# Optimization experiments

Hardware: AMD Instinct MI355X
Metric: run time of the kernel (lower is better)

Reference implementation:

```python
import jax, jax.numpy as jnp
import numpy as np


def setup_inputs() -> dict:
    key = jax.random.key(0)
    B, D, F = 8192, 768, 32768
    k_x, k_w = jax.random.split(key, 2)
    x = jax.random.normal(k_x, (B, D), dtype=jnp.float32)
    # xavier_normal init for W_enc: std = sqrt(2/(fan_in+fan_out))
    scale = (2.0 / (D + F)) ** 0.5
    W_enc = jax.random.normal(k_w, (D, F), dtype=jnp.float32) * scale
    # W_dec = W_enc.T with unit-norm rows (latent directions)
    W_dec = W_enc.T
    W_dec = W_dec / jnp.linalg.norm(W_dec, axis=1, keepdims=True)
    pre_bias = jnp.zeros((D,), dtype=jnp.float32)
    latent_bias = jnp.zeros((F,), dtype=jnp.float32)
    return {"x": x, "pre_bias": pre_bias, "W_enc": W_enc,
            "latent_bias": latent_bias, "W_dec": W_dec, "k": 32}


def reference(x, pre_bias, W_enc, latent_bias, W_dec, k):
    # encode: [B,F]
    latents_pre_act = (x - pre_bias) @ W_enc + latent_bias
    # topk selection then relu: relu(topk(pre_act, k))
    vals, idx = jax.lax.top_k(latents_pre_act, k)      # [B,k]
    vals = jax.nn.relu(vals)
    # sparse decode: gather only the k selected decoder rows per example
    # W_dec[idx]: [B,k,D]
    recons = jnp.einsum('bk,bkd->bd', vals, W_dec[idx]) + pre_bias
    return recons
```

## Files before the change

### kernel.cpp

```cpp
#include <hip/hip_runtime.h>
#include <stdint.h>

#define GAS __attribute__((address_space(1)))
#define LAS __attribute__((address_space(3)))

typedef __attribute__((ext_vector_type(8))) short bf16x8;
typedef __attribute__((ext_vector_type(4))) float f32x4;

static constexpr int NB = 8192;
static constexpr int DD = 768;
static constexpr int FF = 32768;
static constexpr int TK = 32;
static constexpr int RUNC = 48;
static constexpr int SLOT = 8;
static constexpr int NSEG = FF / 128;
static constexpr int SORTN = 1024;
static constexpr int NS2 = 256;
static constexpr int NKT = DD / 32;
static constexpr int PQ = 256 * 32;

__device__ __forceinline__ ushort f2bf(float f) {
    unsigned x = __float_as_uint(f);
    unsigned r = (x + 0x7FFFu + ((x >> 16) & 1u)) >> 16;
    return (ushort)r;
}
__device__ __forceinline__ ushort sortkey(ushort u) {
    return (u & 0x8000u) ? (ushort)(u ^ 0xFFFFu) : (ushort)(u | 0x8000u);
}
__device__ __forceinline__ float bf2f(ushort u) {
    return __uint_as_float(((unsigned)u) << 16);
}
__device__ __forceinline__ void gload_lds16(const void* g, void* l) {
    __builtin_amdgcn_global_load_lds((const GAS unsigned int*)g,
                                     (LAS unsigned int*)l, 16, 0, 0);
}
__device__ __forceinline__ size_t pan_off(int v, int d) {
    return ((size_t)(v >> 8) * NKT + (d >> 5)) * PQ + ((v & 255) << 5) + (d & 31);
}

__global__ __launch_bounds__(256) void prep_x_k(const float* __restrict__ x,
                                                const float* __restrict__ pb,
                                                ushort* __restrict__ Ap) {
    const int n4 = NB * DD / 4;
    for (int i = blockIdx.x * 256 + threadIdx.x; i < n4; i += gridDim.x * 256) {
        int b = i / (DD / 4), dq = (i % (DD / 4)) * 4;
        float4 v = ((const float4*)x)[i];
        float4 p = ((const float4*)pb)[i % (DD / 4)];
        ushort4 o;
        o.x = f2bf(v.x - p.x); o.y = f2bf(v.y - p.y);
        o.z = f2bf(v.z - p.z); o.w = f2bf(v.w - p.w);
        *(ushort4*)(Ap + pan_off(b, dq)) = o;
    }
}

__global__ __launch_bounds__(256) void prep_w_k(const float* __restrict__ W,
                                                ushort* __restrict__ Bp,
                                                float* __restrict__ Wt32,
                                                float* __restrict__ s2part) {
    __shared__ float tile[32][33];
    int f0 = blockIdx.x * 32, d0 = blockIdx.y * 32;
    int tx = threadIdx.x & 31, ty = threadIdx.x >> 5;
    float ss = 0.f;
#pragma unroll
    for (int q = 0; q < 4; q++) {
        int dl = ty + q * 8;
        float v = W[(size_t)(d0 + dl) * FF + f0 + tx];
        tile[dl][tx] = v;
        ss += v * v;
    }
#pragma unroll
    for (int o = 32; o >= 1; o >>= 1) ss += __shfl_down(ss, o);
    if ((threadIdx.x & 63) == 0) {
        int slot = (blockIdx.x * 97 + blockIdx.y * 13 + (threadIdx.x >> 6)) & (NS2 - 1);
        atomicAdd(&s2part[slot], ss);
    }
    __syncthreads();
#pragma unroll
    for (int q = 0; q < 4; q++) {
        int fl = ty + q * 8;
        float v = tile[tx][fl];
        int f = f0 + fl, d = d0 + tx;
        Bp[pan_off(f, d)] = f2bf(v);
        if (Wt32) Wt32[(size_t)f * DD + d] = v;
    }
}

__global__ __launch_bounds__(256) void rn_k(const float* __restrict__ x,
                                            const float* __restrict__ pb,
                                            const float* __restrict__ s2part,
                                            float* __restrict__ tau) {
    int t = threadIdx.x, l = t & 63, w = t >> 6;
    __shared__ float wsum[4];
    __shared__ float s2m;
    float p = s2part[t];
#pragma unroll
    for (int o = 32; o >= 1; o >>= 1) p += __shfl_down(p, o);
    if (l == 0) wsum[w] = p;
    __syncthreads();
    if (t == 0) s2m = (wsum[0] + wsum[1] + wsum[2] + wsum[3]) / ((float)DD * (float)FF);
    __syncthreads();
    int row = blockIdx.x * 4 + w;
    float ss = 0.f;
#pragma unroll
    for (int q = 0; q < 12; q++) {
        int d = l + 64 * q;
        float v = x[(size_t)row * DD + d] - pb[d];
        ss += v * v;
    }
#pragma unroll
    for (int o = 32; o >= 1; o >>= 1) ss += __shfl_down(ss, o);
    if (l == 0) tau[row] = 2.5f * sqrtf(s2m * ss);
}

__global__ __launch_bounds__(512, 2) void gemm_k(const ushort* __restrict__ Ap,
                                                 const ushort* __restrict__ Bp,
                                                 const float* __restrict__ lbias,
                                                 const float* __restrict__ tau,
                                                 unsigned* __restrict__ cand,
                                                 unsigned* __restrict__ rowbad) {
    __shared__ __align__(16) char smem[98304];

    int bid = (int)blockIdx.x;
    int wg = (bid & 7) * 512 + (bid >> 3);
    int mt = wg >> 7, nt = wg & 127;
    int m0 = mt << 8, n0 = nt << 8;

    int t = threadIdx.x, l = t & 63, w = t >> 6;
    int wm = w >> 2, wn = w & 3;

    const ushort* sA = Ap + (size_t)mt * NKT * PQ + t * 8;
    const ushort* sB = Bp + (size_t)nt * NKT * PQ + t * 8;
    int ldA = t * 16, ldB = 16384 + t * 16;

    int aro = (wm * 128 + (l & 15)) * 64 + ((l >> 4) << 4);
    int bro = (wn * 64 + (l & 15)) * 64 + ((l >> 4) << 4);

    f32x4 acc[8][4] = {};

#define STAGE(slot, kt)                                                       \
    {                                                                         \
        const size_t o = (size_t)(kt) * PQ;                                   \
        char* base = smem + (slot) * 32768;                                   \
        gload_lds16(sA + o, base + ldA);                                      \
        gload_lds16(sA + o + 4096, base + ldA + 8192);                        \
        gload_lds16(sB + o, base + ldB);                                      \
        gload_lds16(sB + o + 4096, base + ldB + 8192);                        \
    }

    STAGE(0, 0)
    STAGE(1, 1)
    asm volatile("s_waitcnt vmcnt(4)" ::: "memory");
    __builtin_amdgcn_s_barrier();
    __builtin_amdgcn_sched_barrier(0);

    int cur = 0;
#pragma unroll 1
    for (int kt = 0; kt < NKT; kt++) {
        const char* As = smem + cur * 32768;
        const char* Bs = As + 16384;
        int nxt = cur + 2; if (nxt >= 3) nxt -= 3;
        if (kt < NKT - 2) STAGE(nxt, kt + 2)

        bf16x8 af[4], bfr[4];
        af[0]  = *(const bf16x8*)(As + aro);
        af[1]  = *(const bf16x8*)(As + aro + 1024);
        af[2]  = *(const bf16x8*)(As + aro + 2048);
        af[3]  = *(const bf16x8*)(As + aro + 3072);
        bfr[0] = *(const bf16x8*)(Bs + bro);
        bfr[1] = *(const bf16x8*)(Bs + bro + 1024);
        bfr[2] = *(const bf16x8*)(Bs + bro + 2048);
        bfr[3] = *(const bf16x8*)(Bs + bro + 3072);
        asm volatile("s_waitcnt lgkmcnt(0)" ::: "memory");
        __builtin_amdgcn_sched_barrier(0);
        __builtin_amdgcn_s_setprio(1);
#pragma unroll
        for (int mi = 0; mi < 4; mi++)
#pragma unroll
            for (int ni = 0; ni < 4; ni++)
                acc[mi][ni] = __builtin_amdgcn_mfma_f32_16x16x32_bf16(
                    af[mi], bfr[ni], acc[mi][ni], 0, 0, 0);
        __builtin_amdgcn_s_setprio(0);
        __builtin_amdgcn_sched_barrier(0);

        af[0] = *(const bf16x8*)(As + aro + 4096);
        af[1] = *(const bf16x8*)(As + aro + 5120);
        af[2] = *(const bf16x8*)(As + aro + 6144);
        af[3] = *(const bf16x8*)(As + aro + 7168);
        asm volatile("s_waitcnt lgkmcnt(0)" ::: "memory");
        __builtin_amdgcn_sched_barrier(0);
        __builtin_amdgcn_s_setprio(1);
#pragma unroll
        for (int mi = 0; mi < 4; mi++)
#pragma unroll
            for (int ni = 0; ni < 4; ni++)
                acc[mi + 4][ni] = __builtin_amdgcn_mfma_f32_16x16x32_bf16(
                    af[mi], bfr[ni], acc[mi + 4][ni], 0, 0, 0);
        __builtin_amdgcn_s_setprio(0);
        __builtin_amdgcn_sched_barrier(0);

        if (kt < NKT - 2)
            asm volatile("s_waitcnt vmcnt(4)" ::: "memory");
        else
            asm volatile("s_waitcnt vmcnt(0)" ::: "memory");
        __builtin_amdgcn_s_barrier();
        __builtin_amdgcn_sched_barrier(0);
        cur = cur + 1; if (cur == 3) cur = 0;
    }
#undef STAGE

    __syncthreads();
    int* lcnt = (int*)smem;
    unsigned* lbuf = (unsigned*)(smem + 2048);
    lcnt[t] = 0;
    __syncthreads();
    float lbv[4]; int fcol[4];
#pragma unroll
    for (int ni = 0; ni < 4; ni++) {
        fcol[ni] = n0 + wn * 64 + ni * 16 + (l & 15);
        lbv[ni] = lbias[fcol[ni]];
    }
    int sh = wn >> 1;
#pragma unroll
    for (int mi = 0; mi < 8; mi++) {
        int rl = wm * 128 + mi * 16 + ((l >> 4) << 2);
        float4 tq = *(const float4*)(tau + m0 + rl);
        float tj[4] = {tq.x, tq.y, tq.z, tq.w};
#pragma unroll
        for (int ni = 0; ni < 4; ni++) {
            f32x4 v4 = acc[mi][ni];
#pragma unroll
            for (int j = 0; j < 4; j++) {
                float v = v4[j] + lbv[ni];
                if (v >= tj[j]) {
                    int idx = ((rl + j) << 1) + sh;
                    int p = atomicAdd(&lcnt[idx], 1);
                    if (p < SLOT)
                        lbuf[idx * SLOT + p] =
                            ((unsigned)sortkey(f2bf(v)) << 16) | (unsigned)(32767 - fcol[ni]);
                }
            }
        }
    }
    __syncthreads();
    {
        int row = t >> 1, sh2 = t & 1;
        int c = lcnt[t];
        int gr = m0 + row;
        if (c > SLOT) { atomicOr(&rowbad[gr], 1u); c = SLOT; }
        unsigned* dstc = cand + (size_t)gr * (NSEG * SLOT) + ((nt << 1) + sh2) * SLOT;
        for (int s2 = 0; s2 < c; s2++) dstc[s2] = lbuf[t * SLOT + s2];
    }
}

__global__ __launch_bounds__(256) void select2_k(const unsigned* __restrict__ cand,
                                                 const unsigned* __restrict__ rowbad,
                                                 unsigned* __restrict__ flagv,
                                                 int* __restrict__ ridx,
                                                 int* __restrict__ runcnt) {
    int b = blockIdx.x, t = threadIdx.x;
    __shared__ unsigned srt[SORTN];
    __shared__ int s_cnt;
    for (int i = t; i < SORTN; i += 256) srt[i] = 0;
    if (t == 0) s_cnt = 0;
    __syncthreads();
    const uint4* src = (const uint4*)(cand + (size_t)b * (NSEG * SLOT));
    for (int i = t; i < NSEG * SLOT / 4; i += 256) {
        uint4 v4 = src[i];
        unsigned d[4] = {v4.x, v4.y, v4.z, v4.w};
#pragma unroll
        for (int q = 0; q < 4; q++)
            if (d[q]) {
                int p = atomicAdd(&s_cnt, 1);
                if (p < SORTN) srt[p] = d[q];
            }
    }
    __syncthreads();
    int cnt = s_cnt;
    int bad = (rowbad[b] != 0u) || cnt < 48 || cnt > SORTN;
    if (t == 0) { flagv[b] = bad; if (bad) runcnt[b] = 0; }
    if (bad) return;
    for (int k = 2; k <= SORTN; k <<= 1) {
        for (int j = k >> 1; j > 0; j >>= 1) {
#pragma unroll
            for (int q = 0; q < SORTN / 256; q++) {
                int i = t + q * 256;
                int ixj = i ^ j;
                if (ixj > i) {
                    unsigned a = srt[i], c2 = srt[ixj];
                    bool sw = ((i & k) == 0) ? (a < c2) : (a > c2);
                    if (sw) { srt[i] = c2; srt[ixj] = a; }
                }
            }
            __syncthreads();
        }
    }
    int nc = cnt < RUNC ? cnt : RUNC;
    if (t < nc) ridx[(size_t)b * RUNC + t] = 32767 - (int)(srt[t] & 0xFFFFu);
    if (t == 0) runcnt[b] = nc;
}

__global__ __launch_bounds__(256) void fb_k(const unsigned* __restrict__ flagv,
                                            const float* __restrict__ x,
                                            const float* __restrict__ pb,
                                            const ushort* __restrict__ Bp,
                                            const float* __restrict__ lb,
                                            int* __restrict__ ridx,
                                            int* __restrict__ runcnt) {
    int b = blockIdx.x;
    if (!flagv[b]) return;
    int t = threadIdx.x;
    __shared__ float xs[DD];
    __shared__ unsigned hist[256];
    __shared__ int s_cb, s_cum, s_T, s_pos;
    for (int i = t; i < DD; i += 256) xs[i] = x[(size_t)b * DD + i] - pb[i];
    hist[t] = 0;
    if (t == 0) s_pos = 0;
    __syncthreads();
    for (int f = t; f < FF; f += 256) {
        float s = 0.f;
        for (int d = 0; d < DD; d++) s += xs[d] * bf2f(Bp[pan_off(f, d)]);
        ushort k = sortkey(f2bf(s + lb[f]));
        atomicAdd(&hist[k >> 8], 1u);
    }
    __syncthreads();
    if (t == 0) {
        int cum = 0, cb2 = 0;
        for (int i = 255; i >= 0; i--) {
            if (cum + (int)hist[i] >= 48) { cb2 = i; break; }
            cum += (int)hist[i];
        }
        s_cb = cb2; s_cum = cum;
    }
    __syncthreads();
    int cb2 = s_cb;
    hist[t] = 0;
    __syncthreads();
    for (int f = t; f < FF; f += 256) {
        float s = 0.f;
        for (int d = 0; d < DD; d++) s += xs[d] * bf2f(Bp[pan_off(f, d)]);
        ushort k = sortkey(f2bf(s + lb[f]));
        if ((int)(k >> 8) == cb2) atomicAdd(&hist[k & 0xFF], 1u);
    }
    __syncthreads();
    if (t == 0) {
        int cum = s_cum, T = cb2 << 8;
        for (int fb2 = 255; fb2 >= 0; fb2--) {
            if (cum + (int)hist[fb2] >= 48) { T = (cb2 << 8) | fb2; break; }
            cum += (int)hist[fb2];
        }
        s_T = T;
    }
    __syncthreads();
    unsigned T = (unsigned)s_T;
    for (int f = t; f < FF; f += 256) {
        float s = 0.f;
        for (int d = 0; d < DD; d++) s += xs[d] * bf2f(Bp[pan_off(f, d)]);
        ushort k = sortkey(f2bf(s + lb[f]));
        if (k >= T) {
            int p = atomicAdd(&s_pos, 1);
            if (p < RUNC) ridx[(size_t)b * RUNC + p] = f;
        }
    }
    __syncthreads();
    if (t == 0) runcnt[b] = s_pos < RUNC ? s_pos : RUNC;
}

__global__ __launch_bounds__(256) void refine_k(const float* __restrict__ x,
                                                const float* __restrict__ pb,
                                                const float* __restrict__ We,
                                                const float* __restrict__ Wt32,
                                                const float* __restrict__ lb,
                                                const int* __restrict__ runidx,
                                                const int* __restrict__ runcnt,
                                                int use_t,
                                                int* __restrict__ sidx,
                                                float* __restrict__ sval) {
    int b = blockIdx.x, t = threadIdx.x, l = t & 63, w = t >> 6;
    __shared__ float xs[DD];
    __shared__ int ci[RUNC];
    __shared__ float cv[RUNC];
    for (int i = t; i < DD; i += 256) xs[i] = x[(size_t)b * DD + i] - pb[i];
    int c = runcnt[b]; if (c > RUNC) c = RUNC;
    if (t < RUNC) cv[t] = -1e30f;
    if (t < c) ci[t] = runidx[(size_t)b * RUNC + t];
    __syncthreads();
    for (int j = w; j < c; j += 4) {
        int f = ci[j];
        double s = 0.0;
        if (use_t) {
            const float* wr = Wt32 + (size_t)f * DD;
#pragma unroll
            for (int q = 0; q < 12; q++)
                s = fma((double)wr[l + 64 * q], (double)xs[l + 64 * q], s);
        } else {
#pragma unroll
            for (int q = 0; q < 12; q++)
                s = fma((double)We[(size_t)(l + 64 * q) * FF + f], (double)xs[l + 64 * q], s);
        }
#pragma unroll
        for (int o = 32; o >= 1; o >>= 1) s += __shfl_down(s, o);
        if (l == 0) cv[j] = (float)(s + (double)lb[f]);
    }
    __syncthreads();
    if (w == 0) {
        float v0 = (l < RUNC) ? cv[l] : -1e30f;
        int i0 = (l < c) ? ci[l] : 0x7FFFFFFF;
        for (int sel = 0; sel < TK; sel++) {
            float bv = v0; int bi = i0;
#pragma unroll
            for (int o = 32; o >= 1; o >>= 1) {
                float ov = __shfl_xor(bv, o);
                int oi = __shfl_xor(bi, o);
                if (ov > bv || (ov == bv && oi < bi)) { bv = ov; bi = oi; }
            }
            if (i0 == bi) v0 = -1e30f;
            if (l == 0) {
                if (bi == 0x7FFFFFFF) { bi = 0; bv = -1e30f; }
                sidx[(size_t)b * TK + sel] = bi;
                sval[(size_t)b * TK + sel] = bv > 0.f ? bv : 0.f;
            }
        }
    }
}

__global__ __launch_bounds__(192) void decode_k(const float* __restrict__ sval,
                                                const int* __restrict__ sidx,
                                                const float* __restrict__ Wd,
                                                const float* __restrict__ pb,
                                                float* __restrict__ out) {
    int b = blockIdx.x, t = threadIdx.x;
    __shared__ float sv[TK];
    __shared__ int si[TK];
    if (t < TK) { sv[t] = sval[(size_t)b * TK + t]; si[t] = sidx[(size_t)b * TK + t]; }
    __syncthreads();
    float4 acc = ((const float4*)pb)[t];
#pragma unroll 4
    for (int j = 0; j < TK; j++) {
        float v = sv[j];
        float4 wv = ((const float4*)(Wd + (size_t)si[j] * DD))[t];
        acc.x += v * wv.x; acc.y += v * wv.y;
        acc.z += v * wv.z; acc.w += v * wv.w;
    }
    ((float4*)out)[(size_t)b * (DD / 4) + t] = acc;
}

extern "C" void kernel_launch(void* const* d_in, const int* in_sizes, int n_in,
                              void* d_out, int out_size, void* d_ws, size_t ws_size,
                              hipStream_t stream) {
    const float* x  = (const float*)d_in[0];
    const float* pb = (const float*)d_in[1];
    const float* We = (const float*)d_in[2];
    const float* lb = (const float*)d_in[3];
    const float* Wd = (const float*)d_in[4];
    float* out = (float*)d_out;
    char* ws = (char*)d_ws;
    (void)in_sizes; (void)n_in; (void)out_size;

    const size_t SZ_AP   = (size_t)NB * DD * 2;
    const size_t SZ_BP   = (size_t)FF * DD * 2;
    const size_t SZ_WT32 = (size_t)FF * DD * 4;
    const size_t SZ_CAND = (size_t)NB * NSEG * SLOT * 4;
    const size_t SZ_TAU  = (size_t)NB * 4;
    const size_t SZ_RIDX = (size_t)NB * RUNC * 4;
    const size_t SZ_RCNT = (size_t)NB * 4;
    const size_t SZ_SIDX = (size_t)NB * TK * 4;
    const size_t SZ_SVAL = (size_t)NB * TK * 4;
    const size_t SZ_CTRL = (size_t)NB * 4 + NS2 * 4 + SZ_CAND;

    size_t need_base = SZ_AP + SZ_BP + SZ_CTRL + (size_t)NB * 4 +
                       SZ_TAU + SZ_RIDX + SZ_RCNT + SZ_SIDX + SZ_SVAL;
    int use_t = (ws_size >= need_base + SZ_WT32) ? 1 : 0;

    size_t off = 0;
    ushort* Ap    = (ushort*)(ws + off); off += SZ_AP;
    ushort* Bp    = (ushort*)(ws + off); off += SZ_BP;
    float*  Wt32  = nullptr;
    if (use_t) { Wt32 = (float*)(ws + off); off += SZ_WT32; }
    char* ctrl0   = (char*)(ws + off);
    unsigned* rowbad = (unsigned*)(ws + off); off += (size_t)NB * 4;
    float* s2part = (float*)(ws + off); off += NS2 * 4;
    unsigned* cand = (unsigned*)(ws + off); off += SZ_CAND;
    size_t ctrl_bytes = (size_t)((ws + off) - ctrl0);
    unsigned* flagv = (unsigned*)(ws + off); off += (size_t)NB * 4;
    float* tau    = (float*)(ws + off); off += SZ_TAU;
    int* ridx     = (int*)(ws + off); off += SZ_RIDX;
    int* rcnt     = (int*)(ws + off); off += SZ_RCNT;
    int* sidx     = (int*)(ws + off); off += SZ_SIDX;
    float* sval   = (float*)(ws + off); off += SZ_SVAL;

    hipMemsetAsync(ctrl0, 0, ctrl_bytes, stream);
    prep_x_k<<<2048, 256, 0, stream>>>(x, pb, Ap);
    prep_w_k<<<dim3(FF / 32, DD / 32), 256, 0, stream>>>(We, Bp, Wt32, s2part);
    rn_k<<<NB / 4, 256, 0, stream>>>(x, pb, s2part, tau);
    gemm_k<<<(NB / 256) * (FF / 256), 512, 0, stream>>>(Ap, Bp, lb, tau, cand, rowbad);
    select2_k<<<NB, 256, 0, stream>>>(cand, rowbad, flagv, ridx, rcnt);
    fb_k<<<NB, 256, 0, stream>>>(flagv, x, pb, Bp, lb, ridx, rcnt);
    refine_k<<<NB, 256, 0, stream>>>(x, pb, We, Wt32, lb, ridx, rcnt, use_t, sidx, sval);
    decode_k<<<NB, 192, 0, stream>>>(sval, sidx, Wd, pb, out);
}
```

Baseline: 1.103 ms.

## Swizzle GEMM LDS tile layout and deepen load pipeline to four stages

The GEMM's global-to-LDS copies now use a per-thread XOR-swizzled source offset. The fragment read addresses apply the matching swizzle, so the 16-byte LDS reads of A and B fragments spread across banks instead of conflicting. The shared-memory ring grows from three to four 32 KB stages, with three tiles prefetched ahead and the vmcnt waits adjusted to match. This trades more LDS per block (128 KB) for fewer bank conflicts and more latency hiding on the global loads.

```diff
diff --git a/kernel.cpp b/kernel.cpp
--- a/kernel.cpp
+++ b/kernel.cpp
@@ -36,6 +36,10 @@
 }
 __device__ __forceinline__ size_t pan_off(int v, int d) {
     return ((size_t)(v >> 8) * NKT + (d >> 5)) * PQ + ((v & 255) << 5) + (d & 31);
+}
+__device__ __forceinline__ int srcoff(int c) {
+    int P = c >> 3, s8 = (c & 7) ^ (P & 7);
+    return ((P << 1) + (s8 >> 2)) * 32 + (s8 & 3) * 8;
 }
 
 __global__ __launch_bounds__(256) void prep_x_k(const float* __restrict__ x,
@@ -118,7 +122,7 @@
                                                  const float* __restrict__ tau,
                                                  unsigned* __restrict__ cand,
                                                  unsigned* __restrict__ rowbad) {
-    __shared__ __align__(16) char smem[98304];
+    __shared__ __align__(16) char smem[131072];
 
     int bid = (int)blockIdx.x;
     int wg = (bid & 7) * 512 + (bid >> 3);
@@ -128,12 +132,16 @@
     int t = threadIdx.x, l = t & 63, w = t >> 6;
     int wm = w >> 2, wn = w & 3;
 
-    const ushort* sA = Ap + (size_t)mt * NKT * PQ + t * 8;
-    const ushort* sB = Bp + (size_t)nt * NKT * PQ + t * 8;
-    int ldA = t * 16, ldB = 16384 + t * 16;
-
-    int aro = (wm * 128 + (l & 15)) * 64 + ((l >> 4) << 4);
-    int bro = (wn * 64 + (l & 15)) * 64 + ((l >> 4) << 4);
+    int so0 = srcoff(t), so1 = srcoff(t + 512);
+    const ushort* sA = Ap + (size_t)mt * NKT * PQ;
+    const ushort* sB = Bp + (size_t)nt * NKT * PQ;
+
+    int r0a = wm * 128 + (l & 15);
+    int s8a = (r0a & 1) * 4 + (l >> 4);
+    int aro = (r0a >> 1) * 128 + ((s8a ^ ((r0a >> 1) & 7)) << 4);
+    int r0b = wn * 64 + (l & 15);
+    int s8b = (r0b & 1) * 4 + (l >> 4);
+    int bro = (r0b >> 1) * 128 + ((s8b ^ ((r0b >> 1) & 7)) << 4);
 
     f32x4 acc[8][4] = {};
 
@@ -141,25 +149,24 @@
     {                                                                         \
         const size_t o = (size_t)(kt) * PQ;                                   \
         char* base = smem + (slot) * 32768;                                   \
-        gload_lds16(sA + o, base + ldA);                                      \
-        gload_lds16(sA + o + 4096, base + ldA + 8192);                        \
-        gload_lds16(sB + o, base + ldB);                                      \
-        gload_lds16(sB + o + 4096, base + ldB + 8192);                        \
+        gload_lds16(sA + o + so0, base + t * 16);                             \
+        gload_lds16(sA + o + so1, base + t * 16 + 8192);                      \
+        gload_lds16(sB + o + so0, base + 16384 + t * 16);                     \
+        gload_lds16(sB + o + so1, base + 16384 + t * 16 + 8192);              \
     }
 
     STAGE(0, 0)
     STAGE(1, 1)
-    asm volatile("s_waitcnt vmcnt(4)" ::: "memory");
+    STAGE(2, 2)
+    asm volatile("s_waitcnt vmcnt(8)" ::: "memory");
     __builtin_amdgcn_s_barrier();
     __builtin_amdgcn_sched_barrier(0);
 
-    int cur = 0;
 #pragma unroll 1
     for (int kt = 0; kt < NKT; kt++) {
-        const char* As = smem + cur * 32768;
+        const char* As = smem + (kt & 3) * 32768;
         const char* Bs = As + 16384;
-        int nxt = cur + 2; if (nxt >= 3) nxt -= 3;
-        if (kt < NKT - 2) STAGE(nxt, kt + 2)
+        if (kt < NKT - 3) STAGE((kt + 3) & 3, kt + 3)
 
         bf16x8 af[4], bfr[4];
         af[0]  = *(const bf16x8*)(As + aro);
@@ -198,13 +205,15 @@
         __builtin_amdgcn_s_setprio(0);
         __builtin_amdgcn_sched_barrier(0);
 
-        if (kt < NKT - 2)
+        int rem = NKT - 2 - kt;
+        if (rem >= 2)
+            asm volatile("s_waitcnt vmcnt(8)" ::: "memory");
+        else if (rem == 1)
             asm volatile("s_waitcnt vmcnt(4)" ::: "memory");
         else
             asm volatile("s_waitcnt vmcnt(0)" ::: "memory");
         __builtin_amdgcn_s_barrier();
         __builtin_amdgcn_sched_barrier(0);
-        cur = cur + 1; if (cur == 3) cur = 0;
     }
 #undef STAGE
 
@@ -465,10 +474,9 @@
     const size_t SZ_RCNT = (size_t)NB * 4;
     const size_t SZ_SIDX = (size_t)NB * TK * 4;
     const size_t SZ_SVAL = (size_t)NB * TK * 4;
-    const size_t SZ_CTRL = (size_t)NB * 4 + NS2 * 4 + SZ_CAND;
-
-    size_t need_base = SZ_AP + SZ_BP + SZ_CTRL + (size_t)NB * 4 +
-                       SZ_TAU + SZ_RIDX + SZ_RCNT + SZ_SIDX + SZ_SVAL;
+
+    size_t need_base = SZ_AP + SZ_BP + ((size_t)NB * 4 + NS2 * 4 + SZ_CAND) +
+                       (size_t)NB * 4 + SZ_TAU + SZ_RIDX + SZ_RCNT + SZ_SIDX + SZ_SVAL;
     int use_t = (ws_size >= need_base + SZ_WT32) ? 1 : 0;
 
     size_t off = 0;
```

After: 1.091 ms. About the same (-1.1%).
